# Kernel tuning notes

Hardware: AMD Instinct MI355X
Metric: run time of the kernel (lower is better)

## Reference

```python
import jax, jax.numpy as jnp
import numpy as np

B, N, F_IN, F_OUT = 64, 1024, 128, 64
NEG_BIG = -9e15


def setup_inputs() -> dict:
    key = jax.random.key(0)
    k1, k2, k3, k4 = jax.random.split(key, 4)
    atoms_vector = jax.random.normal(k1, (B, N, F_IN), dtype=jnp.float32)
    adjacency = jax.random.randint(k2, (B, N, N), 0, 2, dtype=jnp.int32)
    # xavier_uniform-ish init for params
    W = jax.random.uniform(k3, (F_IN, F_OUT), dtype=jnp.float32, minval=-1.0, maxval=1.0) * (1.414 * np.sqrt(6.0 / (F_IN + F_OUT)))
    a = jax.random.uniform(k4, (2 * F_OUT, 1), dtype=jnp.float32, minval=-1.0, maxval=1.0) * (1.414 * np.sqrt(6.0 / (2 * F_OUT + 1)))
    return {"atoms_vector": atoms_vector, "adjacency": adjacency, "W": W, "a": a}


def reference(atoms_vector, adjacency, W, a):
    f_out = W.shape[1]
    Wh = jnp.einsum('bni,io->bno', atoms_vector, W)  # (B, N, F_OUT)
    # The repeat_interleave/cat construction computes e[b,i,j] =
    # leaky_relu(a1 . Wh[b,i] + a2 . Wh[b,j]) — separable, so compute it directly.
    a1 = a[:f_out, 0]   # (F_OUT,)
    a2 = a[f_out:, 0]   # (F_OUT,)
    s1 = Wh @ a1        # (B, N)
    s2 = Wh @ a2        # (B, N)
    e = jax.nn.leaky_relu(s1[:, :, None] + s2[:, None, :], negative_slope=0.1)  # (B,N,N)
    attention = jnp.where(adjacency > 0, e, jnp.float32(NEG_BIG))
    attention = jax.nn.softmax(attention, axis=2)
    h_prime = jnp.einsum('bij,bjf->bif', attention, Wh)  # (B, N, F_OUT)
    return jax.nn.elu(h_prime)
```

## Files before the change

### kernel.cpp

```cpp
#include <hip/hip_runtime.h>
#include <hip/hip_bf16.h>

#define NN   1024
#define FIN  128
#define FOUT 64
#define TJ   128
#define PSTR 272

typedef __attribute__((ext_vector_type(8))) short short8;
typedef __attribute__((ext_vector_type(4))) float f32x4;

__device__ inline unsigned short f2bf(float x) {
    union { __hip_bfloat16 h; unsigned short u; } c;
    c.h = __float2bfloat16(x);
    return c.u;
}
__device__ inline unsigned packbf(float a, float b) {
    return (unsigned)f2bf(a) | ((unsigned)f2bf(b) << 16);
}

__global__ __launch_bounds__(256) void k1_proj(
    const float* __restrict__ X, const float* __restrict__ W,
    const float* __restrict__ a,
    unsigned short* __restrict__ whbt,
    float* __restrict__ s1g, float* __restrict__ s2g)
{
    __shared__ float Ws[FIN][FOUT];
    __shared__ float Xs[64][FIN + 4];
    __shared__ unsigned short Ob[FOUT][64];

    const int t = threadIdx.x;
    const int blk = blockIdx.x;
    const int b = blk >> 4;
    const int r0 = (blk & 15) << 6;
    const float* Xg = X + ((size_t)(b * NN + r0)) * FIN;

    const float4* Wg4 = (const float4*)W;
    #pragma unroll
    for (int i = 0; i < 8; ++i) {
        int idx = t + i * 256;
        float4 v = Wg4[idx];
        int kk = idx >> 4, oo = (idx & 15) << 2;
        *(float4*)&Ws[kk][oo] = v;
    }
    #pragma unroll
    for (int i = 0; i < 8; ++i) {
        int idx = t + i * 256;
        float4 v = ((const float4*)Xg)[idx];
        int rr = idx >> 5, cc = (idx & 31) << 2;
        *(float4*)&Xs[rr][cc] = v;
    }
    __syncthreads();

    const int l = t & 63, w = t >> 6;
    const int c0 = (l & 15) << 2;
    const int rs = l >> 4;
    const int rbase = w * 16 + rs * 4;

    float acc[4][4] = {};
    for (int k = 0; k < FIN; ++k) {
        float4 wv = *(const float4*)&Ws[k][c0];
        #pragma unroll
        for (int q = 0; q < 4; ++q) {
            float x = Xs[rbase + q][k];
            acc[q][0] += x * wv.x; acc[q][1] += x * wv.y;
            acc[q][2] += x * wv.z; acc[q][3] += x * wv.w;
        }
    }

    float a1v[4], a2v[4];
    #pragma unroll
    for (int c = 0; c < 4; ++c) { a1v[c] = a[c0 + c]; a2v[c] = a[FOUT + c0 + c]; }
    #pragma unroll
    for (int q = 0; q < 4; ++q) {
        float p1 = acc[q][0]*a1v[0] + acc[q][1]*a1v[1] + acc[q][2]*a1v[2] + acc[q][3]*a1v[3];
        float p2 = acc[q][0]*a2v[0] + acc[q][1]*a2v[1] + acc[q][2]*a2v[2] + acc[q][3]*a2v[3];
        #pragma unroll
        for (int m = 1; m <= 8; m <<= 1) {
            p1 += __shfl_xor(p1, m, 64);
            p2 += __shfl_xor(p2, m, 64);
        }
        if ((l & 15) == 0) {
            int row = r0 + rbase + q;
            s1g[b * NN + row] = p1;
            s2g[b * NN + row] = p2;
        }
    }

    #pragma unroll
    for (int q = 0; q < 4; ++q)
        #pragma unroll
        for (int c = 0; c < 4; ++c)
            Ob[c0 + c][rbase + q] = f2bf(acc[q][c]);
    __syncthreads();

    {
        int o = t >> 2, rseg = (t & 3) << 4;
        unsigned short* dst = whbt + ((size_t)(b * FOUT + o)) * NN + r0 + rseg;
        const unsigned short* sp = &Ob[o][rseg];
        *(float4*)dst       = *(const float4*)sp;
        *(float4*)(dst + 8) = *(const float4*)(sp + 8);
    }
}

__global__ __launch_bounds__(256) void k1b_max(
    const float* __restrict__ s2g, float* __restrict__ s2max)
{
    int b = blockIdx.x, t = threadIdx.x;
    float m = -3.4e38f;
    #pragma unroll
    for (int i = 0; i < 4; ++i) m = fmaxf(m, s2g[b * NN + t + i * 256]);
    #pragma unroll
    for (int d = 1; d <= 32; d <<= 1) m = fmaxf(m, __shfl_xor(m, d, 64));
    __shared__ float red[4];
    if ((t & 63) == 0) red[t >> 6] = m;
    __syncthreads();
    if (t == 0) s2max[b] = fmaxf(fmaxf(red[0], red[1]), fmaxf(red[2], red[3]));
}

__global__ __launch_bounds__(256, 4) void k2_attn(
    const int* __restrict__ adj,
    const unsigned short* __restrict__ whbt,
    const float* __restrict__ s1g, const float* __restrict__ s2g,
    const float* __restrict__ s2maxg,
    float* __restrict__ outg)
{
    __shared__ __align__(16) unsigned char Plds[64 * PSTR];
    __shared__ __align__(16) unsigned char Wtl [64 * PSTR];
    __shared__ float lden[64];

    const int t = threadIdx.x;
    const int l = t & 63, w = t >> 6;
    const int bid = blockIdx.x;
    const int b = bid >> 4;
    const int i0 = (bid & 15) << 6;

    const float s2m = s2maxg[b];
    const int halfsel = l >> 5;

    float s1v[8], Mr[8];
    #pragma unroll
    for (int i = 0; i < 8; ++i) {
        float s1 = s1g[b * NN + i0 + w * 16 + 2 * i + halfsel];
        s1v[i] = s1;
        float tt = s1 + s2m;
        Mr[i] = fmaxf(tt, 0.1f * tt);
    }

    const int so = t >> 2, sjq = (t & 3) << 2;
    const unsigned short* wsrc = whbt + ((size_t)(b * FOUT + so)) * NN;
    unsigned char* wdst = Wtl + so * PSTR + sjq * 16;

    const int* adjb = adj + (size_t)b * NN * NN;
    const int jl = (l & 31) << 2;

    float lacc[8];
    #pragma unroll
    for (int i = 0; i < 8; ++i) lacc[i] = 0.f;
    f32x4 acc[4];
    #pragma unroll
    for (int s = 0; s < 4; ++s)
        #pragma unroll
        for (int r = 0; r < 4; ++r) acc[s][r] = 0.f;

    for (int jt = 0; jt < NN; jt += TJ) {
        short8 wreg[4];
        #pragma unroll
        for (int c = 0; c < 4; ++c)
            wreg[c] = *(const short8*)(wsrc + jt + (sjq + c) * 8);

        float4 s2v = *(const float4*)(s2g + b * NN + jt + jl);

        #pragma unroll
        for (int batch = 0; batch < 2; ++batch) {
            int4 av[4];
            #pragma unroll
            for (int ii = 0; ii < 4; ++ii) {
                int i = batch * 4 + ii;
                int ri = w * 16 + 2 * i + halfsel;
                av[ii] = *(const int4*)(adjb + (size_t)(i0 + ri) * NN + jt + jl);
            }
            #pragma unroll
            for (int ii = 0; ii < 4; ++ii) {
                int i = batch * 4 + ii;
                int ri = w * 16 + 2 * i + halfsel;
                float x0 = s1v[i] + s2v.x, x1 = s1v[i] + s2v.y;
                float x2 = s1v[i] + s2v.z, x3 = s1v[i] + s2v.w;
                float e0 = fmaxf(x0, 0.1f * x0), e1 = fmaxf(x1, 0.1f * x1);
                float e2 = fmaxf(x2, 0.1f * x2), e3 = fmaxf(x3, 0.1f * x3);
                float p0 = __expf(e0 - Mr[i]), p1 = __expf(e1 - Mr[i]);
                float p2 = __expf(e2 - Mr[i]), p3 = __expf(e3 - Mr[i]);
                p0 = av[ii].x > 0 ? p0 : 0.f;
                p1 = av[ii].y > 0 ? p1 : 0.f;
                p2 = av[ii].z > 0 ? p2 : 0.f;
                p3 = av[ii].w > 0 ? p3 : 0.f;
                lacc[i] += (p0 + p1) + (p2 + p3);
                uint2 pk = make_uint2(packbf(p0, p1), packbf(p2, p3));
                *(uint2*)(Plds + ri * PSTR + jl * 2) = pk;
            }
        }
        #pragma unroll
        for (int c = 0; c < 4; ++c)
            *(short8*)(wdst + c * 16) = wreg[c];
        __syncthreads();

        const int arow = w * 16 + (l & 15);
        const int ky = (l >> 4) << 4;
        #pragma unroll
        for (int kc = 0; kc < 4; ++kc) {
            short8 af = *(const short8*)(Plds + arow * PSTR + kc * 64 + ky);
            #pragma unroll
            for (int s = 0; s < 4; ++s) {
                short8 bf = *(const short8*)(Wtl + (s * 16 + (l & 15)) * PSTR + kc * 64 + ky);
                acc[s] = __builtin_amdgcn_mfma_f32_16x16x32_bf16(af, bf, acc[s], 0, 0, 0);
            }
        }
        __syncthreads();
    }

    #pragma unroll
    for (int i = 0; i < 8; ++i) {
        float v = lacc[i];
        #pragma unroll
        for (int d = 1; d <= 16; d <<= 1) v += __shfl_xor(v, d, 64);
        lacc[i] = v;
    }
    if ((l & 31) == 0) {
        #pragma unroll
        for (int i = 0; i < 8; ++i) lden[w * 16 + 2 * i + halfsel] = lacc[i];
    }
    __syncthreads();

    const int colg = l & 15;
    const int rbase = (l >> 4) << 2;
    float inv[4];
    #pragma unroll
    for (int r = 0; r < 4; ++r) {
        float ld = lden[w * 16 + rbase + r];
        inv[r] = ld > 0.f ? 1.f / ld : 0.f;
    }
    #pragma unroll
    for (int s = 0; s < 4; ++s)
        #pragma unroll
        for (int r = 0; r < 4; ++r) {
            float v = acc[s][r] * inv[r];
            float res = v > 0.f ? v : (__expf(v) - 1.f);
            outg[((size_t)(b * NN + i0 + w * 16 + rbase + r)) * FOUT + s * 16 + colg] = res;
        }
}

extern "C" void kernel_launch(void* const* d_in, const int* in_sizes, int n_in,
                              void* d_out, int out_size, void* d_ws, size_t ws_size,
                              hipStream_t stream) {
    const float* atoms = (const float*)d_in[0];
    const int*   adj   = (const int*)d_in[1];
    const float* W     = (const float*)d_in[2];
    const float* a     = (const float*)d_in[3];
    float* out = (float*)d_out;

    unsigned short* whbt = (unsigned short*)d_ws;
    float* s1g    = (float*)((char*)d_ws + (8u << 20));
    float* s2g    = (float*)((char*)d_ws + (8u << 20) + (256u << 10));
    float* s2maxg = (float*)((char*)d_ws + (8u << 20) + (512u << 10));

    k1_proj<<<1024, 256, 0, stream>>>(atoms, W, a, whbt, s1g, s2g);
    k1b_max<<<64, 256, 0, stream>>>(s2g, s2maxg);
    k2_attn<<<1024, 256, 0, stream>>>(adj, whbt, s1g, s2g, s2maxg, out);
}
```

Measured before the change: 117.8 us.

## Compute attention probabilities directly in MFMA fragment registers, drop LDS staging

```diff
diff --git a/kernel.cpp b/kernel.cpp
--- a/kernel.cpp
+++ b/kernel.cpp
@@ -4,8 +4,6 @@
 #define NN   1024
 #define FIN  128
 #define FOUT 64
-#define TJ   128
-#define PSTR 272
 
 typedef __attribute__((ext_vector_type(8))) short short8;
 typedef __attribute__((ext_vector_type(4))) float f32x4;
@@ -118,134 +116,88 @@
     if (t == 0) s2max[b] = fmaxf(fmaxf(red[0], red[1]), fmaxf(red[2], red[3]));
 }
 
-__global__ __launch_bounds__(256, 4) void k2_attn(
+__global__ __launch_bounds__(256) void k2_attn(
     const int* __restrict__ adj,
     const unsigned short* __restrict__ whbt,
     const float* __restrict__ s1g, const float* __restrict__ s2g,
     const float* __restrict__ s2maxg,
     float* __restrict__ outg)
 {
-    __shared__ __align__(16) unsigned char Plds[64 * PSTR];
-    __shared__ __align__(16) unsigned char Wtl [64 * PSTR];
-    __shared__ float lden[64];
-
-    const int t = threadIdx.x;
-    const int l = t & 63, w = t >> 6;
+    const int t = threadIdx.x, l = t & 63, w = t >> 6;
     const int bid = blockIdx.x;
     const int b = bid >> 4;
     const int i0 = (bid & 15) << 6;
+    const int r16 = l & 15;
+    const int jo = (l >> 4) << 3;
+    const int row = i0 + w * 16 + r16;
 
     const float s2m = s2maxg[b];
-    const int halfsel = l >> 5;
-
-    float s1v[8], Mr[8];
-    #pragma unroll
-    for (int i = 0; i < 8; ++i) {
-        float s1 = s1g[b * NN + i0 + w * 16 + 2 * i + halfsel];
-        s1v[i] = s1;
-        float tt = s1 + s2m;
-        Mr[i] = fmaxf(tt, 0.1f * tt);
-    }
-
-    const int so = t >> 2, sjq = (t & 3) << 2;
-    const unsigned short* wsrc = whbt + ((size_t)(b * FOUT + so)) * NN;
-    unsigned char* wdst = Wtl + so * PSTR + sjq * 16;
-
-    const int* adjb = adj + (size_t)b * NN * NN;
-    const int jl = (l & 31) << 2;
-
-    float lacc[8];
-    #pragma unroll
-    for (int i = 0; i < 8; ++i) lacc[i] = 0.f;
+    const float s1v = s1g[b * NN + row];
+    const float tt = s1v + s2m;
+    const float Mr = fmaxf(tt, 0.1f * tt);
+
+    const int* adjr = adj + (size_t)b * NN * NN + (size_t)row * NN;
+    const float* s2r = s2g + b * NN;
+    const unsigned short* wb = whbt + (size_t)b * FOUT * NN + (size_t)r16 * NN;
+
     f32x4 acc[4];
     #pragma unroll
     for (int s = 0; s < 4; ++s)
         #pragma unroll
         for (int r = 0; r < 4; ++r) acc[s][r] = 0.f;
-
-    for (int jt = 0; jt < NN; jt += TJ) {
-        short8 wreg[4];
-        #pragma unroll
-        for (int c = 0; c < 4; ++c)
-            wreg[c] = *(const short8*)(wsrc + jt + (sjq + c) * 8);
-
-        float4 s2v = *(const float4*)(s2g + b * NN + jt + jl);
-
-        #pragma unroll
-        for (int batch = 0; batch < 2; ++batch) {
-            int4 av[4];
-            #pragma unroll
-            for (int ii = 0; ii < 4; ++ii) {
-                int i = batch * 4 + ii;
-                int ri = w * 16 + 2 * i + halfsel;
-                av[ii] = *(const int4*)(adjb + (size_t)(i0 + ri) * NN + jt + jl);
-            }
-            #pragma unroll
-            for (int ii = 0; ii < 4; ++ii) {
-                int i = batch * 4 + ii;
-                int ri = w * 16 + 2 * i + halfsel;
-                float x0 = s1v[i] + s2v.x, x1 = s1v[i] + s2v.y;
-                float x2 = s1v[i] + s2v.z, x3 = s1v[i] + s2v.w;
-                float e0 = fmaxf(x0, 0.1f * x0), e1 = fmaxf(x1, 0.1f * x1);
-                float e2 = fmaxf(x2, 0.1f * x2), e3 = fmaxf(x3, 0.1f * x3);
-                float p0 = __expf(e0 - Mr[i]), p1 = __expf(e1 - Mr[i]);
-                float p2 = __expf(e2 - Mr[i]), p3 = __expf(e3 - Mr[i]);
-                p0 = av[ii].x > 0 ? p0 : 0.f;
-                p1 = av[ii].y > 0 ? p1 : 0.f;
-                p2 = av[ii].z > 0 ? p2 : 0.f;
-                p3 = av[ii].w > 0 ? p3 : 0.f;
-                lacc[i] += (p0 + p1) + (p2 + p3);
-                uint2 pk = make_uint2(packbf(p0, p1), packbf(p2, p3));
-                *(uint2*)(Plds + ri * PSTR + jl * 2) = pk;
-            }
-        }
-        #pragma unroll
-        for (int c = 0; c < 4; ++c)
-            *(short8*)(wdst + c * 16) = wreg[c];
-        __syncthreads();
-
-        const int arow = w * 16 + (l & 15);
-        const int ky = (l >> 4) << 4;
-        #pragma unroll
-        for (int kc = 0; kc < 4; ++kc) {
-            short8 af = *(const short8*)(Plds + arow * PSTR + kc * 64 + ky);
-            #pragma unroll
-            for (int s = 0; s < 4; ++s) {
-                short8 bf = *(const short8*)(Wtl + (s * 16 + (l & 15)) * PSTR + kc * 64 + ky);
-                acc[s] = __builtin_amdgcn_mfma_f32_16x16x32_bf16(af, bf, acc[s], 0, 0, 0);
-            }
-        }
-        __syncthreads();
-    }
-
-    #pragma unroll
-    for (int i = 0; i < 8; ++i) {
-        float v = lacc[i];
-        #pragma unroll
-        for (int d = 1; d <= 16; d <<= 1) v += __shfl_xor(v, d, 64);
-        lacc[i] = v;
-    }
-    if ((l & 31) == 0) {
-        #pragma unroll
-        for (int i = 0; i < 8; ++i) lden[w * 16 + 2 * i + halfsel] = lacc[i];
-    }
-    __syncthreads();
-
-    const int colg = l & 15;
-    const int rbase = (l >> 4) << 2;
+    float den = 0.f;
+
+    #pragma unroll 2
+    for (int jt = 0; jt < NN; jt += 32) {
+        const int j0 = jt + jo;
+        int4 a0 = *(const int4*)(adjr + j0);
+        int4 a1 = *(const int4*)(adjr + j0 + 4);
+        float4 sa = *(const float4*)(s2r + j0);
+        float4 sb = *(const float4*)(s2r + j0 + 4);
+        short8 bf[4];
+        #pragma unroll
+        for (int s = 0; s < 4; ++s)
+            bf[s] = *(const short8*)(wb + (size_t)s * (16 * NN) + j0);
+
+        const float sv[8] = {sa.x, sa.y, sa.z, sa.w, sb.x, sb.y, sb.z, sb.w};
+        const int   am[8] = {a0.x, a0.y, a0.z, a0.w, a1.x, a1.y, a1.z, a1.w};
+        unsigned pk[4];
+        #pragma unroll
+        for (int e = 0; e < 4; ++e) {
+            float xa = s1v + sv[2*e];
+            float xb = s1v + sv[2*e+1];
+            float ea = fmaxf(xa, 0.1f * xa) - Mr;
+            float eb = fmaxf(xb, 0.1f * xb) - Mr;
+            float pa = am[2*e]   > 0 ? __expf(ea) : 0.f;
+            float pb = am[2*e+1] > 0 ? __expf(eb) : 0.f;
+            den += pa + pb;
+            pk[e] = packbf(pa, pb);
+        }
+        union { unsigned u[4]; short8 s8; } A;
+        A.u[0] = pk[0]; A.u[1] = pk[1]; A.u[2] = pk[2]; A.u[3] = pk[3];
+        #pragma unroll
+        for (int s = 0; s < 4; ++s)
+            acc[s] = __builtin_amdgcn_mfma_f32_16x16x32_bf16(A.s8, bf[s], acc[s], 0, 0, 0);
+    }
+
+    den += __shfl_xor(den, 16, 64);
+    den += __shfl_xor(den, 32, 64);
+
+    const int rb = (l >> 4) << 2;
     float inv[4];
     #pragma unroll
-    for (int r = 0; r < 4; ++r) {
-        float ld = lden[w * 16 + rbase + r];
-        inv[r] = ld > 0.f ? 1.f / ld : 0.f;
-    }
+    for (int rr = 0; rr < 4; ++rr) {
+        float dd = __shfl(den, rb + rr, 64);
+        inv[rr] = dd > 0.f ? 1.f / dd : 0.f;
+    }
+    float* orow = outg + ((size_t)(b * NN + i0 + w * 16 + rb)) * FOUT;
     #pragma unroll
     for (int s = 0; s < 4; ++s)
         #pragma unroll
-        for (int r = 0; r < 4; ++r) {
-            float v = acc[s][r] * inv[r];
+        for (int rr = 0; rr < 4; ++rr) {
+            float v = acc[s][rr] * inv[rr];
             float res = v > 0.f ? v : (__expf(v) - 1.f);
-            outg[((size_t)(b * NN + i0 + w * 16 + rbase + r)) * FOUT + s * 16 + colg] = res;
+            orow[(size_t)rr * FOUT + s * 16 + r16] = res;
         }
 }
 
```

Result: slower. 127.8 us (+8.5%).
